# Optimization experiments

Hardware: AMD Instinct MI355X
Metric: run time of the kernel (lower is better)

Reference implementation:

```python
import jax, jax.numpy as jnp
import numpy as np

P = 3; C = 64; IMG = 48; G = IMG // P
D = C * P * P          # 576 embedding dim == flatten dim
NH = 12; HD = D // NH  # 48 head dim
HID = 4 * D            # 2304
NL = 4; S = G * G      # 256 patches
NQ = 6
QN, QP = -8.0, 7.0     # 4-bit signed LSQ range
EPS = 1e-5


def lsq(w):
    # LSQ fake-quant of weights, step size from LSQ init formula, STE rounding
    alpha = 2.0 * jnp.mean(jnp.abs(w)) / jnp.sqrt(QP)
    q = jnp.clip(w / alpha, QN, QP)
    q = q + jax.lax.stop_gradient(jnp.round(q) - q)
    return q * alpha


def qlinear(x, w, b=None):
    y = x @ lsq(w).T
    return y if b is None else y + b


def ln(x, g, b):
    m = jnp.mean(x, -1, keepdims=True)
    v = jnp.var(x, -1, keepdims=True)
    return (x - m) / jnp.sqrt(v + EPS) * g + b


def mha(q, k, v, in_w, out_w):
    # q,k,v: [S,B,D]; in_w: [3D,D]; out_w: [D,D]; no biases
    Wq, Wk, Wv = jnp.split(lsq(in_w), 3, axis=0)
    def heads(t, W):
        return (t @ W.T).reshape(t.shape[0], t.shape[1], NH, HD)
    qh = heads(q, Wq) * (1.0 / jnp.sqrt(HD))
    kh = heads(k, Wk)
    vh = heads(v, Wv)
    att = jax.nn.softmax(jnp.einsum('qbhd,kbhd->bhqk', qh, kh), axis=-1)
    o = jnp.einsum('bhqk,kbhd->qbhd', att, vh).reshape(q.shape[0], q.shape[1], D)
    return o @ lsq(out_w).T


def _forward(x, lin_enc_w, lin_enc_b, pos_emb, query_embed_w,
             enc_in_w, enc_out_w, enc_l1_w, enc_l1_b, enc_l2_w, enc_l2_b,
             enc_ln1_g, enc_ln1_b, enc_ln2_g, enc_ln2_b,
             dec_sa_in_w, dec_sa_out_w, dec_ca_in_w, dec_ca_out_w,
             dec_l1_w, dec_l1_b, dec_l2_w, dec_l2_b,
             dec_ln1_g, dec_ln1_b, dec_ln2_g, dec_ln2_b, dec_ln3_g, dec_ln3_b,
             head1_w, head1_b, head2_w, head2_b, query_idx):
    B = x.shape[0]
    # unfold -> [S,B,flat], channel-major patch flattening like F.unfold
    t = x.reshape(B, C, G, P, G, P).transpose(0, 1, 3, 5, 2, 4)
    t = t.reshape(B, C * P * P, G * G).transpose(2, 0, 1)  # [S,B,D]
    t = qlinear(t, lin_enc_w, lin_enc_b) + t
    qe = query_embed_w[query_idx].reshape(S, 1, D)   # query_pos, broadcasts over B
    pos = pos_emb[:, None, :]                        # [S,1,D]
    h = t + pos
    for l in range(NL):  # encoder (pre-norm)
        h2 = ln(h, enc_ln1_g[l], enc_ln1_b[l])
        h = h + mha(h2, h2, h2, enc_in_w[l], enc_out_w[l])
        h2 = ln(h, enc_ln2_g[l], enc_ln2_b[l])
        h = h + qlinear(jax.nn.relu(qlinear(h2, enc_l1_w[l], enc_l1_b[l])), enc_l2_w[l], enc_l2_b[l])
    mem = h
    o = mem
    for l in range(NL):  # decoder, memory = encoder output
        o2 = ln(o, dec_ln1_g[l], dec_ln1_b[l])
        qk = o2 + qe
        o = o + mha(qk, qk, o2, dec_sa_in_w[l], dec_sa_out_w[l])
        o2 = ln(o, dec_ln2_g[l], dec_ln2_b[l])
        o = o + mha(o2 + qe, mem, mem, dec_ca_in_w[l], dec_ca_out_w[l])
        o2 = ln(o, dec_ln3_g[l], dec_ln3_b[l])
        o = o + qlinear(jax.nn.relu(qlinear(o2, dec_l1_w[l], dec_l1_b[l])), dec_l2_w[l], dec_l2_b[l])
    # mlp_head with residual
    o = o + qlinear(jax.nn.relu(qlinear(o, head1_w, head1_b)), head2_w, head2_b)
    # fold back: [S,B,D] -> [B,C,IMG,IMG]
    y = o.transpose(1, 2, 0).reshape(B, C, P, P, G, G).transpose(0, 1, 4, 2, 5, 3)
    return y.reshape(B, C, IMG, IMG)


def setup_inputs() -> dict:
    key = jax.random.key(0)
    ks = iter(jax.random.split(key, 64))
    def w(shape):
        return jax.random.normal(next(ks), shape, jnp.float32) * 0.02
    B = 4
    inp = {
        'x': jax.random.normal(next(ks), (B, C, IMG, IMG), jnp.float32),
        'lin_enc_w': w((D, D)), 'lin_enc_b': jnp.zeros((D,), jnp.float32),
        'pos_emb': w((S, D)),
        'query_embed_w': w((NQ, S * D)),
        'enc_in_w': w((NL, 3 * D, D)), 'enc_out_w': w((NL, D, D)),
        'enc_l1_w': w((NL, HID, D)), 'enc_l1_b': jnp.zeros((NL, HID), jnp.float32),
        'enc_l2_w': w((NL, D, HID)), 'enc_l2_b': jnp.zeros((NL, D), jnp.float32),
        'enc_ln1_g': jnp.ones((NL, D), jnp.float32), 'enc_ln1_b': jnp.zeros((NL, D), jnp.float32),
        'enc_ln2_g': jnp.ones((NL, D), jnp.float32), 'enc_ln2_b': jnp.zeros((NL, D), jnp.float32),
        'dec_sa_in_w': w((NL, 3 * D, D)), 'dec_sa_out_w': w((NL, D, D)),
        'dec_ca_in_w': w((NL, 3 * D, D)), 'dec_ca_out_w': w((NL, D, D)),
        'dec_l1_w': w((NL, HID, D)), 'dec_l1_b': jnp.zeros((NL, HID), jnp.float32),
        'dec_l2_w': w((NL, D, HID)), 'dec_l2_b': jnp.zeros((NL, D), jnp.float32),
        'dec_ln1_g': jnp.ones((NL, D), jnp.float32), 'dec_ln1_b': jnp.zeros((NL, D), jnp.float32),
        'dec_ln2_g': jnp.ones((NL, D), jnp.float32), 'dec_ln2_b': jnp.zeros((NL, D), jnp.float32),
        'dec_ln3_g': jnp.ones((NL, D), jnp.float32), 'dec_ln3_b': jnp.zeros((NL, D), jnp.float32),
        'head1_w': w((HID, D)), 'head1_b': jnp.zeros((HID,), jnp.float32),
        'head2_w': w((D, HID)), 'head2_b': jnp.zeros((D,), jnp.float32),
        'query_idx': 0,
    }
    return inp


def reference(x, lin_enc_w, lin_enc_b, pos_emb, query_embed_w,
              enc_in_w, enc_out_w, enc_l1_w, enc_l1_b, enc_l2_w, enc_l2_b,
              enc_ln1_g, enc_ln1_b, enc_ln2_g, enc_ln2_b,
              dec_sa_in_w, dec_sa_out_w, dec_ca_in_w, dec_ca_out_w,
              dec_l1_w, dec_l1_b, dec_l2_w, dec_l2_b,
              dec_ln1_g, dec_ln1_b, dec_ln2_g, dec_ln2_b, dec_ln3_g, dec_ln3_b,
              head1_w, head1_b, head2_w, head2_b, query_idx):
    return _forward(x, lin_enc_w, lin_enc_b, pos_emb, query_embed_w,
                    enc_in_w, enc_out_w, enc_l1_w, enc_l1_b, enc_l2_w, enc_l2_b,
                    enc_ln1_g, enc_ln1_b, enc_ln2_g, enc_ln2_b,
                    dec_sa_in_w, dec_sa_out_w, dec_ca_in_w, dec_ca_out_w,
                    dec_l1_w, dec_l1_b, dec_l2_w, dec_l2_b,
                    dec_ln1_g, dec_ln1_b, dec_ln2_g, dec_ln2_b, dec_ln3_g, dec_ln3_b,
                    head1_w, head1_b, head2_w, head2_b, query_idx)
```

## Files before the change

kernel.cpp:

```cpp
#include <hip/hip_runtime.h>
#include <cstddef>

#define Pp    3
#define Cc    64
#define IMGi  48
#define Gg    16
#define Dd    576
#define NHh   12
#define HDd   48
#define HIDh  2304
#define NLl   4
#define Ss    256
#define Bb    4
#define Mm    1024
#define EPSf  1e-5f
#define NJOBS 43

typedef short short8 __attribute__((ext_vector_type(8)));
typedef short short4v __attribute__((ext_vector_type(4)));
typedef float f32x4  __attribute__((ext_vector_type(4)));

struct QJobs { const float* ptr[NJOBS]; int n[NJOBS]; int off[NJOBS]; };

__device__ __forceinline__ short f2bf(float f) {
  unsigned u = __float_as_uint(f);
  u = u + 0x7fffu + ((u >> 16) & 1u);
  return (short)(u >> 16);
}

typedef __attribute__((address_space(3))) unsigned lds_u32;
typedef __attribute__((address_space(1))) const unsigned glob_u32;
__device__ __forceinline__ void gload_lds16(const void* g, void* l) {
  __builtin_amdgcn_global_load_lds((glob_u32*)g, (lds_u32*)l, 16, 0, 0);
}


__global__ void k_zero(float* p, int n) {
  int i = blockIdx.x * blockDim.x + threadIdx.x;
  if (i < n) p[i] = 0.f;
}

__global__ void k_abssum(QJobs jobs, float* absum) {
  int job = blockIdx.x >> 6, blk = blockIdx.x & 63;
  const float* p = jobs.ptr[job];
  int n4 = jobs.n[job] >> 2;
  float s = 0.f;
  for (int i = blk * 256 + threadIdx.x; i < n4; i += 64 * 256) {
    float4 v = *(const float4*)(p + (size_t)i * 4);
    s += fabsf(v.x) + fabsf(v.y) + fabsf(v.z) + fabsf(v.w);
  }
  __shared__ float red[256];
  red[threadIdx.x] = s; __syncthreads();
  for (int o = 128; o > 0; o >>= 1) {
    if (threadIdx.x < o) red[threadIdx.x] += red[threadIdx.x + o];
    __syncthreads();
  }
  if (threadIdx.x == 0) atomicAdd(&absum[job], red[0]);
}

__global__ void k_alpha(QJobs jobs, const float* absum, float* alpha, float* inva) {
  int j = threadIdx.x;
  if (j < NJOBS) {
    float a = 2.f * (absum[j] / (float)jobs.n[j]) / sqrtf(7.f);
    alpha[j] = a;
    inva[j] = 1.f / a;
  }
}

__global__ void k_quant(QJobs jobs, const float* __restrict__ inva, short* __restrict__ wq) {
  int job = blockIdx.x >> 7, blk = blockIdx.x & 127;
  const float* p = jobs.ptr[job];
  int n8 = jobs.n[job] >> 3;
  short* dst = wq + (size_t)jobs.off[job];
  float ia = inva[job];
  for (int i = blk * 256 + threadIdx.x; i < n8; i += 128 * 256) {
    const float4* p4 = (const float4*)(p + (size_t)i * 8);
    float4 w0 = p4[0], w1 = p4[1];
    short8 bv;
    bv[0] = f2bf(rintf(fminf(7.f, fmaxf(-8.f, w0.x * ia))));
    bv[1] = f2bf(rintf(fminf(7.f, fmaxf(-8.f, w0.y * ia))));
    bv[2] = f2bf(rintf(fminf(7.f, fmaxf(-8.f, w0.z * ia))));
    bv[3] = f2bf(rintf(fminf(7.f, fmaxf(-8.f, w0.w * ia))));
    bv[4] = f2bf(rintf(fminf(7.f, fmaxf(-8.f, w1.x * ia))));
    bv[5] = f2bf(rintf(fminf(7.f, fmaxf(-8.f, w1.y * ia))));
    bv[6] = f2bf(rintf(fminf(7.f, fmaxf(-8.f, w1.z * ia))));
    bv[7] = f2bf(rintf(fminf(7.f, fmaxf(-8.f, w1.w * ia))));
    *(short8*)(dst + (size_t)i * 8) = bv;
  }
}

__global__ void k_patchify(const float* __restrict__ x, float* __restrict__ t) {
  int i = blockIdx.x * 256 + threadIdx.x;
  if (i >= Mm * Dd) return;
  int d = i % Dd, row = i / Dd;
  int b = row % Bb, s = row / Bb;
  int c = d / 9, r = d % 9;
  int p1 = r / 3, p2 = r % 3;
  int g1 = s / Gg, g2 = s % Gg;
  t[i] = x[((size_t)(b * Cc + c) * IMGi + (g1 * Pp + p1)) * IMGi + (g2 * Pp + p2)];
}

__global__ void k_unpatch(const float* __restrict__ h, float* __restrict__ out) {
  int i = blockIdx.x * 256 + threadIdx.x;
  if (i >= Bb * Cc * IMGi * IMGi) return;
  int j = i % IMGi, t = i / IMGi;
  int r = t % IMGi; t /= IMGi;
  int c = t % Cc;
  int b = t / Cc;
  int g1 = r / Pp, p1 = r % Pp, g2 = j / Pp, p2 = j % Pp;
  int s = g1 * Gg + g2;
  int d = c * 9 + p1 * 3 + p2;
  out[i] = h[(size_t)(s * Bb + b) * Dd + d];
}

__global__ __launch_bounds__(256)
void k_ln(const float* __restrict__ x, const float* __restrict__ g,
          const float* __restrict__ b, float* __restrict__ y) {
  int w = threadIdx.x >> 6, lane = threadIdx.x & 63;
  int row = blockIdx.x * 4 + w;
  const float* xr = x + (size_t)row * Dd;
  float v[9];
  float s = 0.f, s2 = 0.f;
  #pragma unroll
  for (int i = 0; i < 9; ++i) {
    v[i] = xr[lane + i * 64];
    s += v[i]; s2 += v[i] * v[i];
  }
  #pragma unroll
  for (int o = 32; o; o >>= 1) { s += __shfl_xor(s, o); s2 += __shfl_xor(s2, o); }
  float mean = s * (1.f / Dd);
  float var  = s2 * (1.f / Dd) - mean * mean;
  float inv  = rsqrtf(var + EPSf);
  float* yr = y + (size_t)row * Dd;
  #pragma unroll
  for (int i = 0; i < 9; ++i) {
    int c = lane + i * 64;
    yr[c] = (v[i] - mean) * inv * g[c] + b[c];
  }
}

#define MT 64
#define NT 64
#define KC 576
#define LDKA 584

__device__ __forceinline__ int bswz(int row, int colByte) {
  return row * 1152 + (colByte ^ ((row & 7) << 4));
}

__global__ __launch_bounds__(256)
void k_gemm_mfma(const float* __restrict__ Xa, const float* __restrict__ Xb,
                 int n_split, int ldx,
                 const float* __restrict__ qe, const int* __restrict__ qidx,
                 const float* __restrict__ Wraw, const short* __restrict__ Wq,
                 const float* __restrict__ bias, const float* __restrict__ pos,
                 const float* res, int ldr,
                 float* out, int ldo, float* out2,
                 int N, int K,
                 const float* __restrict__ alpha_p, const float* __restrict__ inva_p,
                 int slot, int relu)
{
  __shared__ short As[MT][LDKA];
  __shared__ short Bs[NT * KC];
  const int tid  = threadIdx.x;
  const int wave = tid >> 6, lane = tid & 63;
  const int quad = lane >> 4, l15 = lane & 15;
  const int tile_m = blockIdx.y * MT, tile_n = blockIdx.x * NT;
  const int m_off = (wave >> 1) * 32, n_off = (wave & 1) * 32;
  const int sr = tid >> 2;
  const int sc = (tid & 3) * 8;
  const float inva = inva_p[slot];

  const float* X = (!Xb || tile_n < n_split) ? Xa : Xb;
  const bool addqe = (qe != nullptr) && (tile_n < n_split);
  size_t qe_off = 0;
  if (addqe) qe_off = (size_t)qidx[0] * ((size_t)Ss * Dd);

  f32x4 acc00 = {0,0,0,0}, acc01 = {0,0,0,0}, acc10 = {0,0,0,0}, acc11 = {0,0,0,0};

  for (int kc = 0; kc < K; kc += KC) {
    if (Wq) {
      #pragma unroll
      for (int j = 0; j < 18; ++j) {
        const int c = wave * 18 + j;
        const int p = c * 512 + lane * 8;
        const int prow  = p / KC;
        const int pcolB = (p % KC) * 2;
        const int lcolB = pcolB ^ ((prow & 7) << 4);
        const short* src = Wq + (size_t)(tile_n + prow) * K + kc + (lcolB >> 1);
        gload_lds16(src, (char*)Bs + c * 1024);
      }
    } else {
      const float* wr = Wraw + (size_t)(tile_n + sr) * K + kc;
      #pragma unroll
      for (int j = 0; j < 18; ++j) {
        const int k = sc + j * 32;
        float4 w0 = *(const float4*)(wr + k);
        float4 w1 = *(const float4*)(wr + k + 4);
        short8 bv;
        bv[0] = f2bf(rintf(fminf(7.f, fmaxf(-8.f, w0.x * inva))));
        bv[1] = f2bf(rintf(fminf(7.f, fmaxf(-8.f, w0.y * inva))));
        bv[2] = f2bf(rintf(fminf(7.f, fmaxf(-8.f, w0.z * inva))));
        bv[3] = f2bf(rintf(fminf(7.f, fmaxf(-8.f, w0.w * inva))));
        bv[4] = f2bf(rintf(fminf(7.f, fmaxf(-8.f, w1.x * inva))));
        bv[5] = f2bf(rintf(fminf(7.f, fmaxf(-8.f, w1.y * inva))));
        bv[6] = f2bf(rintf(fminf(7.f, fmaxf(-8.f, w1.z * inva))));
        bv[7] = f2bf(rintf(fminf(7.f, fmaxf(-8.f, w1.w * inva))));
        *(short8*)((char*)Bs + bswz(sr, k * 2)) = bv;
      }
    }

    {
      const float* ar = X + (size_t)(tile_m + sr) * ldx + kc;
      const float* qr = addqe ? (qe + qe_off + (size_t)((tile_m + sr) >> 2) * Dd + kc)
                              : nullptr;
      #pragma unroll 6
      for (int j = 0; j < 18; ++j) {
        const int k = sc + j * 32;
        float4 a0 = *(const float4*)(ar + k);
        float4 a1 = *(const float4*)(ar + k + 4);
        if (addqe) {
          float4 q0 = *(const float4*)(qr + k);
          float4 q1 = *(const float4*)(qr + k + 4);
          a0.x += q0.x; a0.y += q0.y; a0.z += q0.z; a0.w += q0.w;
          a1.x += q1.x; a1.y += q1.y; a1.z += q1.z; a1.w += q1.w;
        }
        short8 av;
        av[0] = f2bf(a0.x); av[1] = f2bf(a0.y); av[2] = f2bf(a0.z); av[3] = f2bf(a0.w);
        av[4] = f2bf(a1.x); av[5] = f2bf(a1.y); av[6] = f2bf(a1.z); av[7] = f2bf(a1.w);
        *(short8*)&As[sr][k] = av;
      }
    }
    __syncthreads();

    #pragma unroll 3
    for (int ks = 0; ks < KC / 32; ++ks) {
      const int kb = ks * 32 + quad * 8;
      short8 af0 = *(short8*)&As[m_off + l15][kb];
      short8 af1 = *(short8*)&As[m_off + 16 + l15][kb];
      short8 bf0 = *(const short8*)((const char*)Bs + bswz(n_off + l15, kb * 2));
      short8 bf1 = *(const short8*)((const char*)Bs + bswz(n_off + 16 + l15, kb * 2));
      acc00 = __builtin_amdgcn_mfma_f32_16x16x32_bf16(af0, bf0, acc00, 0, 0, 0);
      acc01 = __builtin_amdgcn_mfma_f32_16x16x32_bf16(af0, bf1, acc01, 0, 0, 0);
      acc10 = __builtin_amdgcn_mfma_f32_16x16x32_bf16(af1, bf0, acc10, 0, 0, 0);
      acc11 = __builtin_amdgcn_mfma_f32_16x16x32_bf16(af1, bf1, acc11, 0, 0, 0);
    }
    __syncthreads();
  }

  const float a_s = alpha_p[slot];
  const int rowb = tile_m + m_off + quad * 4;
  const int colb = tile_n + n_off + l15;
  f32x4 accs[4] = {acc00, acc01, acc10, acc11};
  #pragma unroll
  for (int t = 0; t < 4; ++t) {
    int row0 = rowb + ((t >> 1) * 16);
    int col  = colb + ((t & 1) * 16);
    float bv = bias ? bias[col] : 0.f;
    #pragma unroll
    for (int r = 0; r < 4; ++r) {
      int row = row0 + r;
      float v = accs[t][r] * a_s + bv;
      if (res) v += res[(size_t)row * ldr + col];
      if (pos) v += pos[(size_t)(row >> 2) * Dd + col];
      if (relu) v = fmaxf(v, 0.f);
      out[(size_t)row * ldo + col] = v;
      if (out2) out2[(size_t)row * ldo + col] = v;
    }
  }
}

__global__ __launch_bounds__(256)
void k_attn(const float* __restrict__ QKV, float* __restrict__ ctx, float scale) {
  __shared__ short Ks[256][72];
  __shared__ short Qs[64][72];
  __shared__ short Vt[48][264];
  __shared__ short Pq[64][264];
  const int qt = blockIdx.x;
  const int b  = blockIdx.y / NHh, h = blockIdx.y % NHh;
  const int tid = threadIdx.x;
  const int w = tid >> 6, lane = tid & 63, quad = lane >> 4, l15 = lane & 15;

  {
    const float* kp = QKV + (size_t)(tid * Bb + b) * 1728 + Dd + h * HDd;
    #pragma unroll
    for (int d0 = 0; d0 < 48; d0 += 4) {
      float4 f = *(const float4*)(kp + d0);
      short4v v = { f2bf(f.x), f2bf(f.y), f2bf(f.z), f2bf(f.w) };
      *(short4v*)&Ks[tid][d0] = v;
    }
    short4v z = {0, 0, 0, 0};
    *(short4v*)&Ks[tid][48] = z; *(short4v*)&Ks[tid][52] = z;
    *(short4v*)&Ks[tid][56] = z; *(short4v*)&Ks[tid][60] = z;
    const float* vp = QKV + (size_t)(tid * Bb + b) * 1728 + 2 * Dd + h * HDd;
    #pragma unroll
    for (int d0 = 0; d0 < 48; d0 += 4) {
      float4 f = *(const float4*)(vp + d0);
      Vt[d0 + 0][tid] = f2bf(f.x);
      Vt[d0 + 1][tid] = f2bf(f.y);
      Vt[d0 + 2][tid] = f2bf(f.z);
      Vt[d0 + 3][tid] = f2bf(f.w);
    }
    if (tid < 64) {
      const float* qp = QKV + (size_t)((qt * 64 + tid) * Bb + b) * 1728 + h * HDd;
      #pragma unroll
      for (int d0 = 0; d0 < 48; d0 += 4) {
        float4 f = *(const float4*)(qp + d0);
        short4v v = { f2bf(f.x), f2bf(f.y), f2bf(f.z), f2bf(f.w) };
        *(short4v*)&Qs[tid][d0] = v;
      }
      *(short4v*)&Qs[tid][48] = z; *(short4v*)&Qs[tid][52] = z;
      *(short4v*)&Qs[tid][56] = z; *(short4v*)&Qs[tid][60] = z;
    }
  }
  __syncthreads();

  short8 bq0 = *(short8*)&Qs[w * 16 + l15][quad * 8];
  short8 bq1 = *(short8*)&Qs[w * 16 + l15][32 + quad * 8];
  f32x4 sf[16];
  #pragma unroll
  for (int mt = 0; mt < 16; ++mt) {
    f32x4 acc = {0, 0, 0, 0};
    short8 a0 = *(short8*)&Ks[mt * 16 + l15][quad * 8];
    short8 a1 = *(short8*)&Ks[mt * 16 + l15][32 + quad * 8];
    acc = __builtin_amdgcn_mfma_f32_16x16x32_bf16(a0, bq0, acc, 0, 0, 0);
    acc = __builtin_amdgcn_mfma_f32_16x16x32_bf16(a1, bq1, acc, 0, 0, 0);
    sf[mt] = acc;
  }

  float mx = -1e30f;
  #pragma unroll
  for (int mt = 0; mt < 16; ++mt)
    #pragma unroll
    for (int r = 0; r < 4; ++r) {
      sf[mt][r] *= scale;
      mx = fmaxf(mx, sf[mt][r]);
    }
  mx = fmaxf(mx, __shfl_xor(mx, 16));
  mx = fmaxf(mx, __shfl_xor(mx, 32));
  float sum = 0.f;
  #pragma unroll
  for (int mt = 0; mt < 16; ++mt)
    #pragma unroll
    for (int r = 0; r < 4; ++r) {
      float e = __expf(sf[mt][r] - mx);
      sf[mt][r] = e;
      sum += e;
    }
  sum += __shfl_xor(sum, 16);
  sum += __shfl_xor(sum, 32);
  float inv = 1.f / sum;

  #pragma unroll
  for (int mt = 0; mt < 16; ++mt) {
    short4v p = { f2bf(sf[mt][0] * inv), f2bf(sf[mt][1] * inv),
                  f2bf(sf[mt][2] * inv), f2bf(sf[mt][3] * inv) };
    *(short4v*)&Pq[w * 16 + l15][mt * 16 + quad * 4] = p;
  }
  __syncthreads();

  f32x4 of0 = {0,0,0,0}, of1 = {0,0,0,0}, of2 = {0,0,0,0};
  #pragma unroll
  for (int kt = 0; kt < 8; ++kt) {
    short8 a = *(short8*)&Pq[w * 16 + l15][kt * 32 + quad * 8];
    short8 b0 = *(short8*)&Vt[l15][kt * 32 + quad * 8];
    short8 b1 = *(short8*)&Vt[16 + l15][kt * 32 + quad * 8];
    short8 b2 = *(short8*)&Vt[32 + l15][kt * 32 + quad * 8];
    of0 = __builtin_amdgcn_mfma_f32_16x16x32_bf16(a, b0, of0, 0, 0, 0);
    of1 = __builtin_amdgcn_mfma_f32_16x16x32_bf16(a, b1, of1, 0, 0, 0);
    of2 = __builtin_amdgcn_mfma_f32_16x16x32_bf16(a, b2, of2, 0, 0, 0);
  }
  const int qg = qt * 64 + w * 16 + quad * 4;
  #pragma unroll
  for (int r = 0; r < 4; ++r) {
    float* cr = ctx + (size_t)((qg + r) * Bb + b) * Dd + h * HDd + l15;
    cr[0]  = of0[r];
    cr[16] = of1[r];
    cr[32] = of2[r];
  }
}


extern "C" void kernel_launch(void* const* d_in, const int* in_sizes, int n_in,
                              void* d_out, int out_size, void* d_ws, size_t ws_size,
                              hipStream_t stream) {
  (void)in_sizes; (void)n_in; (void)out_size;
  const float* x            = (const float*)d_in[0];
  const float* lin_enc_w    = (const float*)d_in[1];
  const float* lin_enc_b    = (const float*)d_in[2];
  const float* pos_emb      = (const float*)d_in[3];
  const float* query_embed  = (const float*)d_in[4];
  const float* enc_in_w     = (const float*)d_in[5];
  const float* enc_out_w    = (const float*)d_in[6];
  const float* enc_l1_w     = (const float*)d_in[7];
  const float* enc_l1_b     = (const float*)d_in[8];
  const float* enc_l2_w     = (const float*)d_in[9];
  const float* enc_l2_b     = (const float*)d_in[10];
  const float* enc_ln1_g    = (const float*)d_in[11];
  const float* enc_ln1_b    = (const float*)d_in[12];
  const float* enc_ln2_g    = (const float*)d_in[13];
  const float* enc_ln2_b    = (const float*)d_in[14];
  const float* dec_sa_in_w  = (const float*)d_in[15];
  const float* dec_sa_out_w = (const float*)d_in[16];
  const float* dec_ca_in_w  = (const float*)d_in[17];
  const float* dec_ca_out_w = (const float*)d_in[18];
  const float* dec_l1_w     = (const float*)d_in[19];
  const float* dec_l1_b     = (const float*)d_in[20];
  const float* dec_l2_w     = (const float*)d_in[21];
  const float* dec_l2_b     = (const float*)d_in[22];
  const float* dec_ln1_g    = (const float*)d_in[23];
  const float* dec_ln1_b    = (const float*)d_in[24];
  const float* dec_ln2_g    = (const float*)d_in[25];
  const float* dec_ln2_b    = (const float*)d_in[26];
  const float* dec_ln3_g    = (const float*)d_in[27];
  const float* dec_ln3_b    = (const float*)d_in[28];
  const float* head1_w      = (const float*)d_in[29];
  const float* head1_b      = (const float*)d_in[30];
  const float* head2_w      = (const float*)d_in[31];
  const float* head2_b      = (const float*)d_in[32];
  const int*   query_idx    = (const int*)d_in[33];
  float* out = (float*)d_out;

  const int DD  = Dd * Dd;
  const int IN3 = 3 * Dd * Dd;
  const int FF  = HIDh * Dd;
  const int MD  = Mm * Dd;

  float* ws = (float*)d_ws;
  float* ABSUM = ws;
  float* ALPHA = ws + 64;
  float* INVA  = ws + 128;
  float* H   = ws + 256;
  float* MEM = H   + MD;
  float* LN  = MEM + MD;
  float* LNQ = LN  + MD;
  float* CTX = LNQ + MD;
  float* QKV = CTX + MD;
  size_t act_floats = 256 + 5 * (size_t)MD + (size_t)Mm * HIDh;
  short* WQ = (short*)(ws + act_floats);
  const size_t WQ_ELEMS = (size_t)DD + 4 * ((size_t)IN3 + DD + FF + FF)
                        + 4 * ((size_t)IN3 + DD + IN3 + DD + FF + FF)
                        + 2 * (size_t)FF;
  const bool use_wq = ws_size >= act_floats * 4 + WQ_ELEMS * 2;

  QJobs jobs;
  int j = 0; int off = 0;
  auto addjob = [&](const float* p, int n) { jobs.ptr[j] = p; jobs.n[j] = n; jobs.off[j] = off; off += n; j++; };
  addjob(lin_enc_w, DD);
  for (int l = 0; l < NLl; ++l) addjob(enc_in_w  + (size_t)l * IN3, IN3);
  for (int l = 0; l < NLl; ++l) addjob(enc_out_w + (size_t)l * DD,  DD);
  for (int l = 0; l < NLl; ++l) addjob(enc_l1_w  + (size_t)l * FF,  FF);
  for (int l = 0; l < NLl; ++l) addjob(enc_l2_w  + (size_t)l * FF,  FF);
  for (int l = 0; l < NLl; ++l) addjob(dec_sa_in_w  + (size_t)l * IN3, IN3);
  for (int l = 0; l < NLl; ++l) addjob(dec_sa_out_w + (size_t)l * DD,  DD);
  for (int l = 0; l < NLl; ++l) addjob(dec_ca_in_w  + (size_t)l * IN3, IN3);
  for (int l = 0; l < NLl; ++l) addjob(dec_ca_out_w + (size_t)l * DD,  DD);
  for (int l = 0; l < NLl; ++l) addjob(dec_l1_w + (size_t)l * FF, FF);
  for (int l = 0; l < NLl; ++l) addjob(dec_l2_w + (size_t)l * FF, FF);
  addjob(head1_w, FF);
  addjob(head2_w, FF);

  k_zero<<<1, 64, 0, stream>>>(ABSUM, 64);
  k_abssum<<<NJOBS * 64, 256, 0, stream>>>(jobs, ABSUM);
  k_alpha<<<1, 64, 0, stream>>>(jobs, ABSUM, ALPHA, INVA);
  if (use_wq) k_quant<<<NJOBS * 128, 256, 0, stream>>>(jobs, INVA, WQ);

  auto gemm = [&](const float* Xa, const float* Xb, int n_split, int ldx,
                  const float* qe,
                  const float* W, int slot, const float* bias, const float* pos,
                  const float* res, int ldr,
                  float* o, int ldo, float* o2, int N, int K, int relu) {
    dim3 grid(N / NT, Mm / MT);
    const short* wq = use_wq ? WQ + (size_t)jobs.off[slot] : nullptr;
    const float* wr = use_wq ? nullptr : W;
    k_gemm_mfma<<<grid, 256, 0, stream>>>(Xa, Xb, n_split, ldx, qe, query_idx,
                                          wr, wq, bias, pos, res, ldr,
                                          o, ldo, o2, N, K, ALPHA, INVA, slot, relu);
  };

  const float scale = 1.f / sqrtf((float)HDd);
  auto attn = [&](const float* out_w, int out_slot) {
    k_attn<<<dim3(Ss / 64, Bb * NHh), 256, 0, stream>>>(QKV, CTX, scale);
    gemm(CTX, nullptr, 0, Dd, nullptr, out_w, out_slot, nullptr, nullptr,
         H, Dd, H, Dd, nullptr, Dd, Dd, 0);
  };

  const int NELEM = Mm * Dd;
  const int EB = (NELEM + 255) / 256;

  k_patchify<<<EB, 256, 0, stream>>>(x, LN);
  gemm(LN, nullptr, 0, Dd, nullptr, lin_enc_w, 0, lin_enc_b, pos_emb,
       LN, Dd, H, Dd, nullptr, Dd, Dd, 0);

  for (int l = 0; l < NLl; ++l) {
    k_ln<<<Mm / 4, 256, 0, stream>>>(H, enc_ln1_g + l * Dd, enc_ln1_b + l * Dd, LN);
    gemm(LN, nullptr, 0, Dd, nullptr, enc_in_w + (size_t)l * IN3, 1 + l,
         nullptr, nullptr, nullptr, 0, QKV, 1728, nullptr, 1728, Dd, 0);
    attn(enc_out_w + (size_t)l * DD, 5 + l);
    k_ln<<<Mm / 4, 256, 0, stream>>>(H, enc_ln2_g + l * Dd, enc_ln2_b + l * Dd, LN);
    gemm(LN, nullptr, 0, Dd, nullptr, enc_l1_w + (size_t)l * FF, 9 + l,
         enc_l1_b + l * HIDh, nullptr, nullptr, 0, QKV, HIDh, nullptr, HIDh, Dd, 1);
    gemm(QKV, nullptr, 0, HIDh, nullptr, enc_l2_w + (size_t)l * FF, 13 + l,
         enc_l2_b + l * Dd, nullptr, H, Dd, H, Dd, (l == NLl - 1) ? MEM : nullptr,
         Dd, HIDh, 0);
  }

  for (int l = 0; l < NLl; ++l) {
    k_ln<<<Mm / 4, 256, 0, stream>>>(H, dec_ln1_g + l * Dd, dec_ln1_b + l * Dd, LN);
    gemm(LN, LN, 2 * Dd, Dd, query_embed, dec_sa_in_w + (size_t)l * IN3, 17 + l,
         nullptr, nullptr, nullptr, 0, QKV, 1728, nullptr, 1728, Dd, 0);
    attn(dec_sa_out_w + (size_t)l * DD, 21 + l);
    k_ln<<<Mm / 4, 256, 0, stream>>>(H, dec_ln2_g + l * Dd, dec_ln2_b + l * Dd, LN);
    gemm(LN, MEM, Dd, Dd, query_embed, dec_ca_in_w + (size_t)l * IN3, 25 + l,
         nullptr, nullptr, nullptr, 0, QKV, 1728, nullptr, 1728, Dd, 0);
    attn(dec_ca_out_w + (size_t)l * DD, 29 + l);
    k_ln<<<Mm / 4, 256, 0, stream>>>(H, dec_ln3_g + l * Dd, dec_ln3_b + l * Dd, LN);
    gemm(LN, nullptr, 0, Dd, nullptr, dec_l1_w + (size_t)l * FF, 33 + l,
         dec_l1_b + l * HIDh, nullptr, nullptr, 0, QKV, HIDh, nullptr, HIDh, Dd, 1);
    gemm(QKV, nullptr, 0, HIDh, nullptr, dec_l2_w + (size_t)l * FF, 37 + l,
         dec_l2_b + l * Dd, nullptr, H, Dd, H, Dd, nullptr, Dd, HIDh, 0);
  }

  gemm(H, nullptr, 0, Dd, nullptr, head1_w, 41, head1_b, nullptr,
       nullptr, 0, QKV, HIDh, nullptr, HIDh, Dd, 1);
  gemm(QKV, nullptr, 0, HIDh, nullptr, head2_w, 42, head2_b, nullptr,
       H, Dd, H, Dd, nullptr, Dd, HIDh, 0);

  k_unpatch<<<EB, 256, 0, stream>>>(H, out);
}
```

Before: 1.550 ms.

## Fuse LayerNorm into GEMM A-tile loads and widen weight quant/abssum kernels

Removes the standalone LayerNorm kernel. Each GEMM block now computes the row mean and variance from its A rows, since K equals the full row, and normalises while staging A into LDS. In the decoder it handles which half of the split input gets normalised. This drops 20 kernel launches and the LN buffer round-trip, but every N-tile block recomputes the statistics and reads A twice. The weight abs-sum reduction also switches to wave shuffles with 4 loads per thread, and the quant kernel processes two chunks per thread.

```diff
diff --git a/kernel.cpp b/kernel.cpp
--- a/kernel.cpp
+++ b/kernel.cpp
@@ -42,20 +42,26 @@
 
 __global__ void k_abssum(QJobs jobs, float* absum) {
   int job = blockIdx.x >> 6, blk = blockIdx.x & 63;
-  const float* p = jobs.ptr[job];
+  const float4* p4 = (const float4*)jobs.ptr[job];
   int n4 = jobs.n[job] >> 2;
-  float s = 0.f;
-  for (int i = blk * 256 + threadIdx.x; i < n4; i += 64 * 256) {
-    float4 v = *(const float4*)(p + (size_t)i * 4);
-    s += fabsf(v.x) + fabsf(v.y) + fabsf(v.z) + fabsf(v.w);
-  }
-  __shared__ float red[256];
-  red[threadIdx.x] = s; __syncthreads();
-  for (int o = 128; o > 0; o >>= 1) {
-    if (threadIdx.x < o) red[threadIdx.x] += red[threadIdx.x + o];
-    __syncthreads();
-  }
-  if (threadIdx.x == 0) atomicAdd(&absum[job], red[0]);
+  float s0 = 0.f, s1 = 0.f, s2 = 0.f, s3 = 0.f;
+  for (int i = blk * 1024 + threadIdx.x; i < n4; i += 64 * 1024) {
+    float4 v = p4[i];
+    s0 += fabsf(v.x) + fabsf(v.y) + fabsf(v.z) + fabsf(v.w);
+    int i1 = i + 256;
+    if (i1 < n4) { float4 w = p4[i1]; s1 += fabsf(w.x) + fabsf(w.y) + fabsf(w.z) + fabsf(w.w); }
+    int i2 = i + 512;
+    if (i2 < n4) { float4 w = p4[i2]; s2 += fabsf(w.x) + fabsf(w.y) + fabsf(w.z) + fabsf(w.w); }
+    int i3 = i + 768;
+    if (i3 < n4) { float4 w = p4[i3]; s3 += fabsf(w.x) + fabsf(w.y) + fabsf(w.z) + fabsf(w.w); }
+  }
+  float s = (s0 + s1) + (s2 + s3);
+  #pragma unroll
+  for (int o = 32; o; o >>= 1) s += __shfl_xor(s, o);
+  __shared__ float red[4];
+  if ((threadIdx.x & 63) == 0) red[threadIdx.x >> 6] = s;
+  __syncthreads();
+  if (threadIdx.x == 0) atomicAdd(&absum[job], (red[0] + red[1]) + (red[2] + red[3]));
 }
 
 __global__ void k_alpha(QJobs jobs, const float* absum, float* alpha, float* inva) {
@@ -73,9 +79,13 @@
   int n8 = jobs.n[job] >> 3;
   short* dst = wq + (size_t)jobs.off[job];
   float ia = inva[job];
-  for (int i = blk * 256 + threadIdx.x; i < n8; i += 128 * 256) {
+  for (int i = blk * 512 + threadIdx.x; i < n8; i += 128 * 512) {
     const float4* p4 = (const float4*)(p + (size_t)i * 8);
     float4 w0 = p4[0], w1 = p4[1];
+    int i1 = i + 256;
+    float4 w2, w3;
+    bool has2 = i1 < n8;
+    if (has2) { const float4* q4 = (const float4*)(p + (size_t)i1 * 8); w2 = q4[0]; w3 = q4[1]; }
     short8 bv;
     bv[0] = f2bf(rintf(fminf(7.f, fmaxf(-8.f, w0.x * ia))));
     bv[1] = f2bf(rintf(fminf(7.f, fmaxf(-8.f, w0.y * ia))));
@@ -86,6 +96,18 @@
     bv[6] = f2bf(rintf(fminf(7.f, fmaxf(-8.f, w1.z * ia))));
     bv[7] = f2bf(rintf(fminf(7.f, fmaxf(-8.f, w1.w * ia))));
     *(short8*)(dst + (size_t)i * 8) = bv;
+    if (has2) {
+      short8 cv;
+      cv[0] = f2bf(rintf(fminf(7.f, fmaxf(-8.f, w2.x * ia))));
+      cv[1] = f2bf(rintf(fminf(7.f, fmaxf(-8.f, w2.y * ia))));
+      cv[2] = f2bf(rintf(fminf(7.f, fmaxf(-8.f, w2.z * ia))));
+      cv[3] = f2bf(rintf(fminf(7.f, fmaxf(-8.f, w2.w * ia))));
+      cv[4] = f2bf(rintf(fminf(7.f, fmaxf(-8.f, w3.x * ia))));
+      cv[5] = f2bf(rintf(fminf(7.f, fmaxf(-8.f, w3.y * ia))));
+      cv[6] = f2bf(rintf(fminf(7.f, fmaxf(-8.f, w3.z * ia))));
+      cv[7] = f2bf(rintf(fminf(7.f, fmaxf(-8.f, w3.w * ia))));
+      *(short8*)(dst + (size_t)i1 * 8) = cv;
+    }
   }
 }
 
@@ -113,32 +135,6 @@
   out[i] = h[(size_t)(s * Bb + b) * Dd + d];
 }
 
-__global__ __launch_bounds__(256)
-void k_ln(const float* __restrict__ x, const float* __restrict__ g,
-          const float* __restrict__ b, float* __restrict__ y) {
-  int w = threadIdx.x >> 6, lane = threadIdx.x & 63;
-  int row = blockIdx.x * 4 + w;
-  const float* xr = x + (size_t)row * Dd;
-  float v[9];
-  float s = 0.f, s2 = 0.f;
-  #pragma unroll
-  for (int i = 0; i < 9; ++i) {
-    v[i] = xr[lane + i * 64];
-    s += v[i]; s2 += v[i] * v[i];
-  }
-  #pragma unroll
-  for (int o = 32; o; o >>= 1) { s += __shfl_xor(s, o); s2 += __shfl_xor(s2, o); }
-  float mean = s * (1.f / Dd);
-  float var  = s2 * (1.f / Dd) - mean * mean;
-  float inv  = rsqrtf(var + EPSf);
-  float* yr = y + (size_t)row * Dd;
-  #pragma unroll
-  for (int i = 0; i < 9; ++i) {
-    int c = lane + i * 64;
-    yr[c] = (v[i] - mean) * inv * g[c] + b[c];
-  }
-}
-
 #define MT 64
 #define NT 64
 #define KC 576
@@ -152,6 +148,8 @@
 void k_gemm_mfma(const float* __restrict__ Xa, const float* __restrict__ Xb,
                  int n_split, int ldx,
                  const float* __restrict__ qe, const int* __restrict__ qidx,
+                 const float* __restrict__ lng, const float* __restrict__ lnb,
+                 int ln_on_b,
                  const float* __restrict__ Wraw, const short* __restrict__ Wq,
                  const float* __restrict__ bias, const float* __restrict__ pos,
                  const float* res, int ldr,
@@ -171,8 +169,10 @@
   const int sc = (tid & 3) * 8;
   const float inva = inva_p[slot];
 
-  const float* X = (!Xb || tile_n < n_split) ? Xa : Xb;
-  const bool addqe = (qe != nullptr) && (tile_n < n_split);
+  const bool isA = (!Xb || tile_n < n_split);
+  const float* X = isA ? Xa : Xb;
+  const bool addqe = (qe != nullptr) && isA;
+  const bool do_ln = isA ? (lng != nullptr) : (ln_on_b != 0);
   size_t qe_off = 0;
   if (addqe) qe_off = (size_t)qidx[0] * ((size_t)Ss * Dd);
 
@@ -211,14 +211,46 @@
     }
 
     {
-      const float* ar = X + (size_t)(tile_m + sr) * ldx + kc;
-      const float* qr = addqe ? (qe + qe_off + (size_t)((tile_m + sr) >> 2) * Dd + kc)
-                              : nullptr;
+      const int arow = tile_m + sr;
+      const float* ar = X + (size_t)arow * ldx + kc;
+      float mean = 0.f, sinv = 1.f;
+      if (do_ln) {
+        float s = 0.f, s2 = 0.f;
+        #pragma unroll 6
+        for (int j = 0; j < 18; ++j) {
+          const int k = sc + j * 32;
+          float4 a0 = *(const float4*)(ar + k);
+          float4 a1 = *(const float4*)(ar + k + 4);
+          s  += (a0.x + a0.y) + (a0.z + a0.w) + (a1.x + a1.y) + (a1.z + a1.w);
+          s2 += (a0.x * a0.x + a0.y * a0.y) + (a0.z * a0.z + a0.w * a0.w)
+              + (a1.x * a1.x + a1.y * a1.y) + (a1.z * a1.z + a1.w * a1.w);
+        }
+        s  += __shfl_xor(s, 1);  s  += __shfl_xor(s, 2);
+        s2 += __shfl_xor(s2, 1); s2 += __shfl_xor(s2, 2);
+        mean = s * (1.f / (float)Dd);
+        float var = s2 * (1.f / (float)Dd) - mean * mean;
+        sinv = rsqrtf(var + EPSf);
+      }
+      const float* qr = addqe ? (qe + qe_off + (size_t)(arow >> 2) * Dd + kc) : nullptr;
       #pragma unroll 6
       for (int j = 0; j < 18; ++j) {
         const int k = sc + j * 32;
         float4 a0 = *(const float4*)(ar + k);
         float4 a1 = *(const float4*)(ar + k + 4);
+        if (do_ln) {
+          float4 g0 = *(const float4*)(lng + kc + k);
+          float4 g1 = *(const float4*)(lng + kc + k + 4);
+          float4 b0 = *(const float4*)(lnb + kc + k);
+          float4 b1 = *(const float4*)(lnb + kc + k + 4);
+          a0.x = (a0.x - mean) * sinv * g0.x + b0.x;
+          a0.y = (a0.y - mean) * sinv * g0.y + b0.y;
+          a0.z = (a0.z - mean) * sinv * g0.z + b0.z;
+          a0.w = (a0.w - mean) * sinv * g0.w + b0.w;
+          a1.x = (a1.x - mean) * sinv * g1.x + b1.x;
+          a1.y = (a1.y - mean) * sinv * g1.y + b1.y;
+          a1.z = (a1.z - mean) * sinv * g1.z + b1.z;
+          a1.w = (a1.w - mean) * sinv * g1.w + b1.w;
+        }
         if (addqe) {
           float4 q0 = *(const float4*)(qr + k);
           float4 q1 = *(const float4*)(qr + k + 4);
@@ -466,7 +498,7 @@
   if (use_wq) k_quant<<<NJOBS * 128, 256, 0, stream>>>(jobs, INVA, WQ);
 
   auto gemm = [&](const float* Xa, const float* Xb, int n_split, int ldx,
-                  const float* qe,
+                  const float* qe, const float* lng, const float* lnb, int lnB,
                   const float* W, int slot, const float* bias, const float* pos,
                   const float* res, int ldr,
                   float* o, int ldo, float* o2, int N, int K, int relu) {
@@ -474,6 +506,7 @@
     const short* wq = use_wq ? WQ + (size_t)jobs.off[slot] : nullptr;
     const float* wr = use_wq ? nullptr : W;
     k_gemm_mfma<<<grid, 256, 0, stream>>>(Xa, Xb, n_split, ldx, qe, query_idx,
+                                          lng, lnb, lnB,
                                           wr, wq, bias, pos, res, ldr,
                                           o, ldo, o2, N, K, ALPHA, INVA, slot, relu);
   };
@@ -481,50 +514,54 @@
   const float scale = 1.f / sqrtf((float)HDd);
   auto attn = [&](const float* out_w, int out_slot) {
     k_attn<<<dim3(Ss / 64, Bb * NHh), 256, 0, stream>>>(QKV, CTX, scale);
-    gemm(CTX, nullptr, 0, Dd, nullptr, out_w, out_slot, nullptr, nullptr,
-         H, Dd, H, Dd, nullptr, Dd, Dd, 0);
+    gemm(CTX, nullptr, 0, Dd, nullptr, nullptr, nullptr, 0, out_w, out_slot,
+         nullptr, nullptr, H, Dd, H, Dd, nullptr, Dd, Dd, 0);
   };
 
   const int NELEM = Mm * Dd;
   const int EB = (NELEM + 255) / 256;
 
   k_patchify<<<EB, 256, 0, stream>>>(x, LN);
-  gemm(LN, nullptr, 0, Dd, nullptr, lin_enc_w, 0, lin_enc_b, pos_emb,
-       LN, Dd, H, Dd, nullptr, Dd, Dd, 0);
+  gemm(LN, nullptr, 0, Dd, nullptr, nullptr, nullptr, 0, lin_enc_w, 0,
+       lin_enc_b, pos_emb, LN, Dd, H, Dd, nullptr, Dd, Dd, 0);
 
   for (int l = 0; l < NLl; ++l) {
-    k_ln<<<Mm / 4, 256, 0, stream>>>(H, enc_ln1_g + l * Dd, enc_ln1_b + l * Dd, LN);
-    gemm(LN, nullptr, 0, Dd, nullptr, enc_in_w + (size_t)l * IN3, 1 + l,
+    gemm(H, nullptr, 0, Dd, nullptr, enc_ln1_g + l * Dd, enc_ln1_b + l * Dd, 0,
+         enc_in_w + (size_t)l * IN3, 1 + l,
          nullptr, nullptr, nullptr, 0, QKV, 1728, nullptr, 1728, Dd, 0);
     attn(enc_out_w + (size_t)l * DD, 5 + l);
-    k_ln<<<Mm / 4, 256, 0, stream>>>(H, enc_ln2_g + l * Dd, enc_ln2_b + l * Dd, LN);
-    gemm(LN, nullptr, 0, Dd, nullptr, enc_l1_w + (size_t)l * FF, 9 + l,
+    gemm(H, nullptr, 0, Dd, nullptr, enc_ln2_g + l * Dd, enc_ln2_b + l * Dd, 0,
+         enc_l1_w + (size_t)l * FF, 9 + l,
          enc_l1_b + l * HIDh, nullptr, nullptr, 0, QKV, HIDh, nullptr, HIDh, Dd, 1);
-    gemm(QKV, nullptr, 0, HIDh, nullptr, enc_l2_w + (size_t)l * FF, 13 + l,
+    gemm(QKV, nullptr, 0, HIDh, nullptr, nullptr, nullptr, 0,
+         enc_l2_w + (size_t)l * FF, 13 + l,
          enc_l2_b + l * Dd, nullptr, H, Dd, H, Dd, (l == NLl - 1) ? MEM : nullptr,
          Dd, HIDh, 0);
   }
 
   for (int l = 0; l < NLl; ++l) {
-    k_ln<<<Mm / 4, 256, 0, stream>>>(H, dec_ln1_g + l * Dd, dec_ln1_b + l * Dd, LN);
-    gemm(LN, LN, 2 * Dd, Dd, query_embed, dec_sa_in_w + (size_t)l * IN3, 17 + l,
+    gemm(H, H, 2 * Dd, Dd, query_embed,
+         dec_ln1_g + l * Dd, dec_ln1_b + l * Dd, 1,
+         dec_sa_in_w + (size_t)l * IN3, 17 + l,
          nullptr, nullptr, nullptr, 0, QKV, 1728, nullptr, 1728, Dd, 0);
     attn(dec_sa_out_w + (size_t)l * DD, 21 + l);
-    k_ln<<<Mm / 4, 256, 0, stream>>>(H, dec_ln2_g + l * Dd, dec_ln2_b + l * Dd, LN);
-    gemm(LN, MEM, Dd, Dd, query_embed, dec_ca_in_w + (size_t)l * IN3, 25 + l,
+    gemm(H, MEM, Dd, Dd, query_embed,
+         dec_ln2_g + l * Dd, dec_ln2_b + l * Dd, 0,
+         dec_ca_in_w + (size_t)l * IN3, 25 + l,
          nullptr, nullptr, nullptr, 0, QKV, 1728, nullptr, 1728, Dd, 0);
     attn(dec_ca_out_w + (size_t)l * DD, 29 + l);
-    k_ln<<<Mm / 4, 256, 0, stream>>>(H, dec_ln3_g + l * Dd, dec_ln3_b + l * Dd, LN);
-    gemm(LN, nullptr, 0, Dd, nullptr, dec_l1_w + (size_t)l * FF, 33 + l,
+    gemm(H, nullptr, 0, Dd, nullptr, dec_ln3_g + l * Dd, dec_ln3_b + l * Dd, 0,
+         dec_l1_w + (size_t)l * FF, 33 + l,
          dec_l1_b + l * HIDh, nullptr, nullptr, 0, QKV, HIDh, nullptr, HIDh, Dd, 1);
-    gemm(QKV, nullptr, 0, HIDh, nullptr, dec_l2_w + (size_t)l * FF, 37 + l,
+    gemm(QKV, nullptr, 0, HIDh, nullptr, nullptr, nullptr, 0,
+         dec_l2_w + (size_t)l * FF, 37 + l,
          dec_l2_b + l * Dd, nullptr, H, Dd, H, Dd, nullptr, Dd, HIDh, 0);
   }
 
-  gemm(H, nullptr, 0, Dd, nullptr, head1_w, 41, head1_b, nullptr,
-       nullptr, 0, QKV, HIDh, nullptr, HIDh, Dd, 1);
-  gemm(QKV, nullptr, 0, HIDh, nullptr, head2_w, 42, head2_b, nullptr,
-       H, Dd, H, Dd, nullptr, Dd, HIDh, 0);
+  gemm(H, nullptr, 0, Dd, nullptr, nullptr, nullptr, 0, head1_w, 41,
+       head1_b, nullptr, nullptr, 0, QKV, HIDh, nullptr, HIDh, Dd, 1);
+  gemm(QKV, nullptr, 0, HIDh, nullptr, nullptr, nullptr, 0, head2_w, 42,
+       head2_b, nullptr, H, Dd, H, Dd, nullptr, Dd, HIDh, 0);
 
   k_unpatch<<<EB, 256, 0, stream>>>(H, out);
 }
```

Result: slower. 1.746 ms (+12.6%).
